# Kernel optimization log

Hardware: AMD Instinct MI355X
Metric: run time of the kernel (lower is better)

## Reference

```python
import jax, jax.numpy as jnp
import numpy as np

B, W = 131072, 32
N_SCEN, SDIM = 19, 16
EMBED_DIM, COMP_DIM = 768, 64
INPUT_DIM = EMBED_DIM + N_SCEN * SDIM  # 1072


def setup_inputs() -> dict:
    key = jax.random.key(0)
    k1, k2, k3, k4, k5, k6 = jax.random.split(key, 6)
    intent_embedding = jax.random.normal(k1, (B, EMBED_DIM), dtype=jnp.float32)
    scenario_ids = jax.random.randint(k2, (B, W), 0, N_SCEN, dtype=jnp.int32)
    # Prefix mask: the torch loop iterates the first int(mask.sum()) slots,
    # so the mask must be a contiguous run of ones.
    lengths = jax.random.randint(k3, (B,), 1, W + 1)
    scenario_mask = (jnp.arange(W)[None, :] < lengths[:, None]).astype(jnp.float32)
    # Parameters (init: normal std=0.01, zero biases)
    scenario_table = 0.01 * jax.random.normal(k4, (N_SCEN, SDIM), dtype=jnp.float32)
    W1 = 0.01 * jax.random.normal(k5, (INPUT_DIM, COMP_DIM), dtype=jnp.float32)
    b1 = jnp.zeros((COMP_DIM,), dtype=jnp.float32)
    W2 = 0.01 * jax.random.normal(k6, (COMP_DIM, 1), dtype=jnp.float32)
    b2 = jnp.zeros((1,), dtype=jnp.float32)
    return {
        "intent_embedding": intent_embedding,
        "scenario_ids": scenario_ids,
        "scenario_mask": scenario_mask,
        "scenario_table": scenario_table,
        "W1": W1, "b1": b1, "W2": W2, "b2": b2,
    }


def reference(intent_embedding, scenario_ids, scenario_mask, scenario_table, W1, b1, W2, b2):
    # Embedding lookup: [B, W, SDIM]
    embeds = scenario_table[scenario_ids]
    masked = embeds * scenario_mask[:, :, None]
    # Vectorized scatter-add into per-scenario bins: [B, N_SCEN, SDIM]
    batch_idx = jnp.arange(scenario_ids.shape[0])[:, None]
    bag3 = jnp.zeros(
        (scenario_ids.shape[0], N_SCEN, SDIM), dtype=embeds.dtype
    ).at[batch_idx, scenario_ids].add(masked)
    counts = scenario_mask.sum(axis=1, keepdims=True)
    bag_vec = bag3.reshape(scenario_ids.shape[0], N_SCEN * SDIM) / jnp.maximum(counts, 1.0)
    combined = jnp.concatenate([intent_embedding, bag_vec], axis=1)  # [B, 1072]
    h = jax.nn.relu(combined @ W1 + b1)  # dropout is identity in eval mode
    return jnp.tanh(h @ W2 + b2)  # [B, 1]
```

## Files before the change

kernel.cpp:

```cpp
#include <hip/hip_runtime.h>
#include <hip/hip_bf16.h>
#include <math.h>

using short8 = __attribute__((ext_vector_type(8))) short;
using f32x4  = __attribute__((ext_vector_type(4))) float;

#define EMB 768
#define CD  64
#define NSCEN 19
#define NCHUNKS (25 * 4)
#define BM 64
#define CHUNK 256
#define ROWP 264

__device__ __forceinline__ ushort f2bf(float x) {
    unsigned u = __float_as_uint(x);
    u += 0x7FFFu + ((u >> 16) & 1u);
    return (ushort)(u >> 16);
}

__device__ __forceinline__ uint cvt2(float x, float y) {
    __hip_bfloat162 h = __float22bfloat162_rn(make_float2(x, y));
    union { __hip_bfloat162 h; uint u; } c;
    c.h = h;
    return c.u;
}

__global__ void prep_W1T(const float* __restrict__ table,
                         const float* __restrict__ W1,
                         ushort* __restrict__ W1T) {
    int e = blockIdx.x * 256 + threadIdx.x;
    if (e >= NCHUNKS * 512) return;
    int chunk = e >> 9, r = e & 511;
    int lane = r >> 3, j = r & 7;
    int ks = chunk >> 2, ct = chunk & 3;
    int col = ct * 16 + (lane & 15);
    int k = ks * 32 + ((lane >> 4) << 3) + j;
    float v = 0.f;
    if (k < EMB) {
        v = W1[(size_t)k * CD + col];
    } else {
        int s = k - EMB;
        if (s < NSCEN) {
            for (int d = 0; d < 16; ++d)
                v += table[s * 16 + d] * W1[(size_t)(EMB + s * 16 + d) * CD + col];
        }
    }
    W1T[e] = f2bf(v);
}

__global__ __launch_bounds__(256, 2)
void scorer_mfma(const float* __restrict__ emb,
                 const int* __restrict__ ids,
                 const float* __restrict__ mask,
                 const ushort* __restrict__ W1T,
                 const float* __restrict__ b1,
                 const float* __restrict__ W2,
                 const float* __restrict__ b2,
                 float* __restrict__ out) {
    __shared__ ushort Abuf[2][BM][ROWP];
    __shared__ float  bagf[BM][21];
    __shared__ ushort bagb[BM][32];

    const int t    = threadIdx.x;
    const int w    = t >> 6;
    const int lane = t & 63;
    const int lr   = lane & 15;
    const int lg   = lane >> 4;
    const int row0 = blockIdx.x * BM;

    float4 sreg[16];
#pragma unroll
    for (int i = 0; i < 16; ++i)
        sreg[i] = *(const float4*)(emb + (size_t)(row0 + i * 4 + w) * EMB + lane * 4);

    for (int e = t; e < BM * 21; e += 256) ((float*)bagf)[e] = 0.f;
    __syncthreads();
    {
        const int r = t >> 2, p = t & 3;
        const int*   idrow = ids  + (size_t)(row0 + r) * 32 + p * 8;
        const float* mrow  = mask + (size_t)(row0 + r) * 32 + p * 8;
        float cnt = 0.f;
#pragma unroll
        for (int q = 0; q < 2; ++q) {
            int4   i4 = ((const int4*)idrow)[q];
            float4 m4 = ((const float4*)mrow)[q];
            atomicAdd(&bagf[r][i4.x], m4.x);
            atomicAdd(&bagf[r][i4.y], m4.y);
            atomicAdd(&bagf[r][i4.z], m4.z);
            atomicAdd(&bagf[r][i4.w], m4.w);
            cnt += m4.x + m4.y + m4.z + m4.w;
        }
        atomicAdd(&bagf[r][20], cnt);
    }
    __syncthreads();
    if (t < BM) {
        float rc = 1.0f / fmaxf(bagf[t][20], 1.0f);
        union { uint u[16]; short8 s[4]; } cv;
#pragma unroll
        for (int p = 0; p < 16; ++p) {
            float x0 = (2 * p     < NSCEN) ? bagf[t][2 * p] * rc     : 0.f;
            float x1 = (2 * p + 1 < NSCEN) ? bagf[t][2 * p + 1] * rc : 0.f;
            cv.u[p] = cvt2(x0, x1);
        }
#pragma unroll
        for (int q = 0; q < 4; ++q) *(short8*)&bagb[t][q * 8] = cv.s[q];
    }

#pragma unroll
    for (int i = 0; i < 16; ++i) {
        uint2 v = make_uint2(cvt2(sreg[i].x, sreg[i].y), cvt2(sreg[i].z, sreg[i].w));
        *(uint2*)&Abuf[0][i * 4 + w][lane * 4] = v;
    }
    __syncthreads();

    const ushort* wp = W1T + (lane << 3);
    f32x4 acc[4];
#pragma unroll
    for (int j = 0; j < 4; ++j) acc[j] = (f32x4)0.f;

    short8 bbA[4], bbB[4];
#define LOADB(dst, kk) do {                                    \
    const ushort* q_ = wp + ((size_t)(kk) << 11);              \
    dst[0] = *(const short8*)(q_);                             \
    dst[1] = *(const short8*)(q_ + 512);                       \
    dst[2] = *(const short8*)(q_ + 1024);                      \
    dst[3] = *(const short8*)(q_ + 1536);                      \
} while (0)

#define MFMA4(a_, b_) do {                                                         \
    acc[0] = __builtin_amdgcn_mfma_f32_16x16x32_bf16(a_, b_[0], acc[0], 0, 0, 0);  \
    acc[1] = __builtin_amdgcn_mfma_f32_16x16x32_bf16(a_, b_[1], acc[1], 0, 0, 0);  \
    acc[2] = __builtin_amdgcn_mfma_f32_16x16x32_bf16(a_, b_[2], acc[2], 0, 0, 0);  \
    acc[3] = __builtin_amdgcn_mfma_f32_16x16x32_bf16(a_, b_[3], acc[3], 0, 0, 0);  \
} while (0)

    LOADB(bbA, 0);

#pragma unroll
    for (int kc = 0; kc < 3; ++kc) {
        const int cb = kc & 1;
        if (kc < 2) {
#pragma unroll
            for (int i = 0; i < 16; ++i)
                sreg[i] = *(const float4*)(emb + (size_t)(row0 + i * 4 + w) * EMB
                                           + (kc + 1) * CHUNK + lane * 4);
        }
#pragma unroll
        for (int ks = 0; ks < 8; ++ks) {
            const int ksg = kc * 8 + ks;
            short8 a = *(const short8*)&Abuf[cb][w * 16 + lr][ks * 32 + lg * 8];
            if ((ks & 1) == 0) {
                LOADB(bbB, ksg + 1);
                MFMA4(a, bbA);
            } else {
                LOADB(bbA, ksg + 1);
                MFMA4(a, bbB);
            }
        }
        if (kc < 2) {
#pragma unroll
            for (int i = 0; i < 16; ++i) {
                uint2 v = make_uint2(cvt2(sreg[i].x, sreg[i].y), cvt2(sreg[i].z, sreg[i].w));
                *(uint2*)&Abuf[cb ^ 1][i * 4 + w][lane * 4] = v;
            }
        }
        __syncthreads();
    }

    {
        short8 ab = *(const short8*)&bagb[w * 16 + lr][lg * 8];
        MFMA4(ab, bbA);
    }

    float b1v[4], w2v[4];
#pragma unroll
    for (int ct = 0; ct < 4; ++ct) {
        int c = ct * 16 + lr;
        b1v[ct] = b1[c];
        w2v[ct] = W2[c];
    }
    const float b2v = b2[0];
#pragma unroll
    for (int r = 0; r < 4; ++r) {
        float p = 0.f;
#pragma unroll
        for (int ct = 0; ct < 4; ++ct) {
            float h = acc[ct][r] + b1v[ct];
            p += fmaxf(h, 0.f) * w2v[ct];
        }
        p += __shfl_xor(p, 1);
        p += __shfl_xor(p, 2);
        p += __shfl_xor(p, 4);
        p += __shfl_xor(p, 8);
        if (lr == 0)
            out[row0 + w * 16 + lg * 4 + r] = tanhf(p + b2v);
    }
#undef LOADB
#undef MFMA4
}

extern "C" void kernel_launch(void* const* d_in, const int* in_sizes, int n_in,
                              void* d_out, int out_size, void* d_ws, size_t ws_size,
                              hipStream_t stream) {
    const float* emb   = (const float*)d_in[0];
    const int*   ids   = (const int*)d_in[1];
    const float* mask  = (const float*)d_in[2];
    const float* table = (const float*)d_in[3];
    const float* W1    = (const float*)d_in[4];
    const float* b1    = (const float*)d_in[5];
    const float* W2    = (const float*)d_in[6];
    const float* b2    = (const float*)d_in[7];
    float* out  = (float*)d_out;
    ushort* W1T = (ushort*)d_ws;

    prep_W1T<<<200, 256, 0, stream>>>(table, W1, W1T);
    const int nblocks = out_size / BM;
    scorer_mfma<<<nblocks, 256, 0, stream>>>(emb, ids, mask, W1T, b1, W2, b2, out);
}
```

Measured before the change: 105.0 us.

## Restructure scorer to 32-row blocks of 512 threads with column-split waves

Blocks shrink to 32 rows with 512 threads. Each of the 8 waves computes one 16-row by 16-column output tile over the full K, so the 64-column reduction now needs an LDS partial-sum buffer and an extra barrier. The whole 32x768 embedding tile is loaded once with nontemporal loads and converted to bf16 in LDS, replacing the three-chunk double-buffered pipeline. The aim is more waves in flight and more memory parallelism for the bandwidth-bound embedding read. In exchange, each wave re-reads A from LDS for only one column tile, and W1T loads are duplicated across waves.

```diff
diff --git a/kernel.cpp b/kernel.cpp
--- a/kernel.cpp
+++ b/kernel.cpp
@@ -4,14 +4,14 @@
 
 using short8 = __attribute__((ext_vector_type(8))) short;
 using f32x4  = __attribute__((ext_vector_type(4))) float;
+using fv4    = __attribute__((ext_vector_type(4))) float;
 
 #define EMB 768
 #define CD  64
 #define NSCEN 19
 #define NCHUNKS (25 * 4)
-#define BM 64
-#define CHUNK 256
-#define ROWP 264
+#define BM 32
+#define ROWP 776
 
 __device__ __forceinline__ ushort f2bf(float x) {
     unsigned u = __float_as_uint(x);
@@ -24,6 +24,11 @@
     union { __hip_bfloat162 h; uint u; } c;
     c.h = h;
     return c.u;
+}
+
+__device__ __forceinline__ float4 ntl4(const float* p) {
+    fv4 v = __builtin_nontemporal_load((const fv4*)p);
+    return make_float4(v[0], v[1], v[2], v[3]);
 }
 
 __global__ void prep_W1T(const float* __restrict__ table,
@@ -49,7 +54,7 @@
     W1T[e] = f2bf(v);
 }
 
-__global__ __launch_bounds__(256, 2)
+__global__ __launch_bounds__(512, 4)
 void scorer_mfma(const float* __restrict__ emb,
                  const int* __restrict__ ids,
                  const float* __restrict__ mask,
@@ -58,146 +63,124 @@
                  const float* __restrict__ W2,
                  const float* __restrict__ b2,
                  float* __restrict__ out) {
-    __shared__ ushort Abuf[2][BM][ROWP];
+    __shared__ ushort Abuf[BM][ROWP];
     __shared__ float  bagf[BM][21];
-    __shared__ ushort bagb[BM][32];
+    __shared__ ushort bagb[BM][40];
+    __shared__ float  part[2][16][4];
 
     const int t    = threadIdx.x;
     const int w    = t >> 6;
     const int lane = t & 63;
     const int lr   = lane & 15;
     const int lg   = lane >> 4;
+    const int rg   = w & 1;
+    const int ct   = w >> 1;
     const int row0 = blockIdx.x * BM;
 
-    float4 sreg[16];
-#pragma unroll
-    for (int i = 0; i < 16; ++i)
-        sreg[i] = *(const float4*)(emb + (size_t)(row0 + i * 4 + w) * EMB + lane * 4);
-
-    for (int e = t; e < BM * 21; e += 256) ((float*)bagf)[e] = 0.f;
-    __syncthreads();
+    float4 sv[12];
     {
-        const int r = t >> 2, p = t & 3;
-        const int*   idrow = ids  + (size_t)(row0 + r) * 32 + p * 8;
-        const float* mrow  = mask + (size_t)(row0 + r) * 32 + p * 8;
-        float cnt = 0.f;
-#pragma unroll
-        for (int q = 0; q < 2; ++q) {
-            int4   i4 = ((const int4*)idrow)[q];
-            float4 m4 = ((const float4*)mrow)[q];
-            atomicAdd(&bagf[r][i4.x], m4.x);
-            atomicAdd(&bagf[r][i4.y], m4.y);
-            atomicAdd(&bagf[r][i4.z], m4.z);
-            atomicAdd(&bagf[r][i4.w], m4.w);
-            cnt += m4.x + m4.y + m4.z + m4.w;
-        }
-        atomicAdd(&bagf[r][20], cnt);
+        const float* src = emb + (size_t)row0 * EMB + (size_t)t * 48;
+#pragma unroll
+        for (int i = 0; i < 12; ++i) sv[i] = ntl4(src + i * 4);
+    }
+    int4 iv; float4 mv;
+    if (t < 256) {
+        const int r = t >> 3, p = t & 7;
+        iv = ((const int4*)(ids + (size_t)(row0 + r) * 32))[p];
+        mv = ((const float4*)(mask + (size_t)(row0 + r) * 32))[p];
+    }
+    const int   ccol = ct * 16 + lr;
+    const float b1v  = b1[ccol];
+    const float w2v  = W2[ccol];
+    const float b2v  = b2[0];
+
+    for (int e = t; e < BM * 21; e += 512) ((float*)bagf)[e] = 0.f;
+    __syncthreads();
+
+    if (t < 256) {
+        const int r = t >> 3;
+        atomicAdd(&bagf[r][iv.x], mv.x);
+        atomicAdd(&bagf[r][iv.y], mv.y);
+        atomicAdd(&bagf[r][iv.z], mv.z);
+        atomicAdd(&bagf[r][iv.w], mv.w);
+        atomicAdd(&bagf[r][20], mv.x + mv.y + mv.z + mv.w);
     }
     __syncthreads();
     if (t < BM) {
         float rc = 1.0f / fmaxf(bagf[t][20], 1.0f);
-        union { uint u[16]; short8 s[4]; } cv;
+        uint u[16];
 #pragma unroll
         for (int p = 0; p < 16; ++p) {
             float x0 = (2 * p     < NSCEN) ? bagf[t][2 * p] * rc     : 0.f;
             float x1 = (2 * p + 1 < NSCEN) ? bagf[t][2 * p + 1] * rc : 0.f;
-            cv.u[p] = cvt2(x0, x1);
+            u[p] = cvt2(x0, x1);
         }
 #pragma unroll
-        for (int q = 0; q < 4; ++q) *(short8*)&bagb[t][q * 8] = cv.s[q];
-    }
-
-#pragma unroll
-    for (int i = 0; i < 16; ++i) {
-        uint2 v = make_uint2(cvt2(sreg[i].x, sreg[i].y), cvt2(sreg[i].z, sreg[i].w));
-        *(uint2*)&Abuf[0][i * 4 + w][lane * 4] = v;
-    }
-    __syncthreads();
-
-    const ushort* wp = W1T + (lane << 3);
-    f32x4 acc[4];
-#pragma unroll
-    for (int j = 0; j < 4; ++j) acc[j] = (f32x4)0.f;
-
-    short8 bbA[4], bbB[4];
-#define LOADB(dst, kk) do {                                    \
-    const ushort* q_ = wp + ((size_t)(kk) << 11);              \
-    dst[0] = *(const short8*)(q_);                             \
-    dst[1] = *(const short8*)(q_ + 512);                       \
-    dst[2] = *(const short8*)(q_ + 1024);                      \
-    dst[3] = *(const short8*)(q_ + 1536);                      \
-} while (0)
-
-#define MFMA4(a_, b_) do {                                                         \
-    acc[0] = __builtin_amdgcn_mfma_f32_16x16x32_bf16(a_, b_[0], acc[0], 0, 0, 0);  \
-    acc[1] = __builtin_amdgcn_mfma_f32_16x16x32_bf16(a_, b_[1], acc[1], 0, 0, 0);  \
-    acc[2] = __builtin_amdgcn_mfma_f32_16x16x32_bf16(a_, b_[2], acc[2], 0, 0, 0);  \
-    acc[3] = __builtin_amdgcn_mfma_f32_16x16x32_bf16(a_, b_[3], acc[3], 0, 0, 0);  \
-} while (0)
-
-    LOADB(bbA, 0);
-
-#pragma unroll
-    for (int kc = 0; kc < 3; ++kc) {
-        const int cb = kc & 1;
-        if (kc < 2) {
-#pragma unroll
-            for (int i = 0; i < 16; ++i)
-                sreg[i] = *(const float4*)(emb + (size_t)(row0 + i * 4 + w) * EMB
-                                           + (kc + 1) * CHUNK + lane * 4);
+        for (int q = 0; q < 4; ++q)
+            *(uint4*)&bagb[t][q * 8] = make_uint4(u[4 * q], u[4 * q + 1], u[4 * q + 2], u[4 * q + 3]);
+    }
+
+    {
+        ushort* dst = &Abuf[t >> 4][(t & 15) * 48];
+#pragma unroll
+        for (int g = 0; g < 3; ++g) {
+            uint u0 = cvt2(sv[4 * g].x,     sv[4 * g].y);
+            uint u1 = cvt2(sv[4 * g].z,     sv[4 * g].w);
+            uint u2 = cvt2(sv[4 * g + 1].x, sv[4 * g + 1].y);
+            uint u3 = cvt2(sv[4 * g + 1].z, sv[4 * g + 1].w);
+            uint u4 = cvt2(sv[4 * g + 2].x, sv[4 * g + 2].y);
+            uint u5 = cvt2(sv[4 * g + 2].z, sv[4 * g + 2].w);
+            uint u6 = cvt2(sv[4 * g + 3].x, sv[4 * g + 3].y);
+            uint u7 = cvt2(sv[4 * g + 3].z, sv[4 * g + 3].w);
+            *(uint4*)(dst + g * 16)     = make_uint4(u0, u1, u2, u3);
+            *(uint4*)(dst + g * 16 + 8) = make_uint4(u4, u5, u6, u7);
         }
-#pragma unroll
-        for (int ks = 0; ks < 8; ++ks) {
-            const int ksg = kc * 8 + ks;
-            short8 a = *(const short8*)&Abuf[cb][w * 16 + lr][ks * 32 + lg * 8];
-            if ((ks & 1) == 0) {
-                LOADB(bbB, ksg + 1);
-                MFMA4(a, bbA);
-            } else {
-                LOADB(bbA, ksg + 1);
-                MFMA4(a, bbB);
-            }
-        }
-        if (kc < 2) {
-#pragma unroll
-            for (int i = 0; i < 16; ++i) {
-                uint2 v = make_uint2(cvt2(sreg[i].x, sreg[i].y), cvt2(sreg[i].z, sreg[i].w));
-                *(uint2*)&Abuf[cb ^ 1][i * 4 + w][lane * 4] = v;
-            }
-        }
-        __syncthreads();
-    }
-
+    }
+    __syncthreads();
+
+    const ushort* wp = W1T + lane * 8;
+    f32x4 acc = (f32x4)0.f;
+    short8 bb[4];
+
+#define LOADB(slot, kk) bb[slot] = *(const short8*)(wp + (((kk) * 4 + ct) << 9))
+
+    LOADB(0, 0); LOADB(1, 1); LOADB(2, 2); LOADB(3, 3);
+#pragma unroll
+    for (int ks = 0; ks < 24; ++ks) {
+        short8 a = *(const short8*)&Abuf[rg * 16 + lr][ks * 32 + lg * 8];
+        acc = __builtin_amdgcn_mfma_f32_16x16x32_bf16(a, bb[ks & 3], acc, 0, 0, 0);
+        if (ks + 4 <= 24) LOADB(ks & 3, ks + 4);
+    }
     {
-        short8 ab = *(const short8*)&bagb[w * 16 + lr][lg * 8];
-        MFMA4(ab, bbA);
-    }
-
-    float b1v[4], w2v[4];
-#pragma unroll
-    for (int ct = 0; ct < 4; ++ct) {
-        int c = ct * 16 + lr;
-        b1v[ct] = b1[c];
-        w2v[ct] = W2[c];
-    }
-    const float b2v = b2[0];
-#pragma unroll
-    for (int r = 0; r < 4; ++r) {
-        float p = 0.f;
-#pragma unroll
-        for (int ct = 0; ct < 4; ++ct) {
-            float h = acc[ct][r] + b1v[ct];
-            p += fmaxf(h, 0.f) * w2v[ct];
-        }
-        p += __shfl_xor(p, 1);
-        p += __shfl_xor(p, 2);
-        p += __shfl_xor(p, 4);
-        p += __shfl_xor(p, 8);
-        if (lr == 0)
-            out[row0 + w * 16 + lg * 4 + r] = tanhf(p + b2v);
+        short8 a = *(const short8*)&bagb[rg * 16 + lr][lg * 8];
+        acc = __builtin_amdgcn_mfma_f32_16x16x32_bf16(a, bb[0], acc, 0, 0, 0);
     }
 #undef LOADB
-#undef MFMA4
+
+    float p0 = 0.f, p1 = 0.f, p2 = 0.f, p3 = 0.f;
+    p0 = fmaxf(acc[0] + b1v, 0.f) * w2v;
+    p1 = fmaxf(acc[1] + b1v, 0.f) * w2v;
+    p2 = fmaxf(acc[2] + b1v, 0.f) * w2v;
+    p3 = fmaxf(acc[3] + b1v, 0.f) * w2v;
+#pragma unroll
+    for (int d = 1; d < 16; d <<= 1) {
+        p0 += __shfl_xor(p0, d);
+        p1 += __shfl_xor(p1, d);
+        p2 += __shfl_xor(p2, d);
+        p3 += __shfl_xor(p3, d);
+    }
+    if (lr == 0) {
+        part[rg][lg * 4 + 0][ct] = p0;
+        part[rg][lg * 4 + 1][ct] = p1;
+        part[rg][lg * 4 + 2][ct] = p2;
+        part[rg][lg * 4 + 3][ct] = p3;
+    }
+    __syncthreads();
+    if (t < BM) {
+        float s = part[t >> 4][t & 15][0] + part[t >> 4][t & 15][1]
+                + part[t >> 4][t & 15][2] + part[t >> 4][t & 15][3];
+        out[row0 + t] = tanhf(s + b2v);
+    }
 }
 
 extern "C" void kernel_launch(void* const* d_in, const int* in_sizes, int n_in,
@@ -216,5 +199,5 @@
 
     prep_W1T<<<200, 256, 0, stream>>>(table, W1, W1T);
     const int nblocks = out_size / BM;
-    scorer_mfma<<<nblocks, 256, 0, stream>>>(emb, ids, mask, W1T, b1, W2, b2, out);
-}
+    scorer_mfma<<<nblocks, 512, 0, stream>>>(emb, ids, mask, W1T, b1, W2, b2, out);
+}
```

Result: slower. 263.4 us (+150.9%).
